# Performance work log

Hardware: AMD Instinct MI355X
Metric: run time of the kernel (lower is better)

The kernel has to match this reference:

```python
import jax, jax.numpy as jnp
import numpy as np

N_NODES = 50000
N_EDGES = 800000


def _layer_norm(h, g, b, eps=1e-5):
    mu = jnp.mean(h, axis=-1, keepdims=True)
    var = jnp.var(h, axis=-1, keepdims=True)
    return (h - mu) * jax.lax.rsqrt(var + eps) * g + b


def _gat_layer(h, src, tgt, trans_prob, W, a_src, a_tgt, Wtp, a_tp, Wskip, b, concat):
    """GATLayerImp3-style edge-softmax attention with transition-prob scores."""
    N = h.shape[0]
    NH, F = a_src.shape
    proj = (h @ W).reshape(N, NH, F)                       # (N, NH, F)
    s_src = jnp.einsum('nhf,hf->nh', proj, a_src)          # (N, NH)
    s_tgt = jnp.einsum('nhf,hf->nh', proj, a_tgt)
    e = s_src[src] + s_tgt[tgt]                            # (E, NH)
    tp_proj = (trans_prob @ Wtp).reshape(-1, NH, F)        # (E, NH, F)
    e = e + jnp.einsum('ehf,hf->eh', tp_proj, a_tp)
    e = jax.nn.leaky_relu(e, 0.2)
    # neighborhood softmax over edges sharing the same target node
    m = jax.ops.segment_max(e, tgt, num_segments=N)        # (N, NH)
    w = jnp.exp(e - m[tgt])
    denom = jax.ops.segment_sum(w, tgt, num_segments=N)
    alpha = w / (denom[tgt] + 1e-16)                       # (E, NH)
    msg = proj[src] * alpha[..., None]                     # (E, NH, F)
    out = jax.ops.segment_sum(msg, tgt, num_segments=N)    # (N, NH, F)
    if Wskip is None:
        out = out + h[:, None, :]                          # F == F_in
    else:
        out = out + (h @ Wskip).reshape(N, NH, F)
    out = out.reshape(N, NH * F) if concat else out.mean(axis=1)
    return jax.nn.elu(out + b)


def setup_inputs() -> dict:
    key = jax.random.key(0)
    ks = jax.random.split(key, 32)
    s = 0.1
    inp = {
        'node_features': jax.random.normal(ks[0], (N_NODES, 128), jnp.float32),
        'edge_index': jax.random.randint(ks[1], (2, N_EDGES), 0, N_NODES, jnp.int32),
        'edge_prob': jax.random.uniform(ks[2], (N_EDGES, 1), jnp.float32),
        'x': jax.random.randint(ks[3], (64, 128), 0, N_NODES, jnp.int32),
        'W0': jax.random.normal(ks[4], (128, 256)) * s,
        'a_src0': jax.random.normal(ks[5], (16, 16)) * s,
        'a_tgt0': jax.random.normal(ks[6], (16, 16)) * s,
        'Wtp0': jax.random.normal(ks[7], (1, 256)) * s,
        'a_tp0': jax.random.normal(ks[8], (16, 16)) * s,
        'Wskip0': jax.random.normal(ks[9], (128, 256)) * s,
        'b0': jnp.zeros((256,)),
        'W1': jax.random.normal(ks[10], (256, 256)) * s,
        'a_src1': jax.random.normal(ks[11], (16, 16)) * s,
        'a_tgt1': jax.random.normal(ks[12], (16, 16)) * s,
        'Wtp1': jax.random.normal(ks[13], (1, 256)) * s,
        'a_tp1': jax.random.normal(ks[14], (16, 16)) * s,
        'Wskip1': jax.random.normal(ks[15], (256, 256)) * s,
        'b1': jnp.zeros((256,)),
        'ln1_g': jnp.ones((256,)),
        'ln1_b': jnp.zeros((256,)),
        'W2': jax.random.normal(ks[16], (256, 256)) * s,
        'a_src2': jax.random.normal(ks[17], (1, 256)) * s,
        'a_tgt2': jax.random.normal(ks[18], (1, 256)) * s,
        'Wtp2': jax.random.normal(ks[19], (1, 256)) * s,
        'a_tp2': jax.random.normal(ks[20], (1, 256)) * s,
        'b2': jnp.zeros((256,)),
        'ln2_g': jnp.ones((256,)),
        'ln2_b': jnp.zeros((256,)),
    }
    return inp


def reference(node_features, edge_index, edge_prob, x,
              W0, a_src0, a_tgt0, Wtp0, a_tp0, Wskip0, b0,
              W1, a_src1, a_tgt1, Wtp1, a_tp1, Wskip1, b1, ln1_g, ln1_b,
              W2, a_src2, a_tgt2, Wtp2, a_tp2, b2, ln2_g, ln2_b):
    src, tgt = edge_index[0], edge_index[1]
    # node encoder GAT layer (concat 16 heads x 16 feats -> 256)
    h = _gat_layer(node_features, src, tgt, edge_prob,
                   W0, a_src0, a_tgt0, Wtp0, a_tp0, Wskip0, b0, concat=True)
    # GM layer 0: GAT (concat) + layer norm
    h = _gat_layer(h, src, tgt, edge_prob,
                   W1, a_src1, a_tgt1, Wtp1, a_tp1, Wskip1, b1, concat=True)
    h = _layer_norm(h, ln1_g, ln1_b)
    # GM layer 1: GAT (avg last, 1 head x 256; skip is identity add) + layer norm
    h = _gat_layer(h, src, tgt, edge_prob,
                   W2, a_src2, a_tgt2, Wtp2, a_tp2, None, b2, concat=False)
    h = _layer_norm(h, ln2_g, ln2_b)
    # indexed gather of node embeddings into per-sequence embeddings
    out = h[x]                                              # (B, S, d_model)
    return out
```

## Files before the change

### kernel.cpp

```cpp
#include <hip/hip_runtime.h>
#include <hip/hip_fp16.h>
#include <math.h>

typedef __attribute__((ext_vector_type(8))) short    s16x8;
typedef __attribute__((ext_vector_type(8))) _Float16 h16x8;
typedef __attribute__((ext_vector_type(4))) float    f32x4;
typedef __attribute__((ext_vector_type(4))) int      i32x4;

__device__ __forceinline__ short f2h(float x){ return __half_as_short(__float2half(x)); }
__device__ __forceinline__ float h2f(short s){ return __half2float(__short_as_half(s)); }

__global__ void k_prep(const float* W0, const float* Ws0, const float* W1,
                       const float* Ws1, const float* W2,
                       short* W0t, short* Ws0t, short* W1t, short* Ws1t, short* W2t,
                       const float* Wtp0, const float* a_tp0,
                       const float* Wtp1, const float* a_tp1,
                       const float* Wtp2, const float* a_tp2, float* cvec,
                       int* counts, int N){
  __shared__ float buf[256];
  int b = blockIdx.x;
  if (b < 1024){
    int idx = b*256 + threadIdx.x;
    const float* W; short* Wt; int K; int base;
    if (idx < 32768)      { W=W0;  Wt=W0t;  K=128; base=0; }
    else if (idx < 65536) { W=Ws0; Wt=Ws0t; K=128; base=32768; }
    else if (idx < 131072){ W=W1;  Wt=W1t;  K=256; base=65536; }
    else if (idx < 196608){ W=Ws1; Wt=Ws1t; K=256; base=131072; }
    else                  { W=W2;  Wt=W2t;  K=256; base=196608; }
    int i = idx - base;
    int n = i / K, k = i - n*K;
    Wt[i] = f2h(W[(size_t)k*256 + n]);
  } else if (b < 1027){
    int layer = b - 1024;
    const float* Wtp = layer==0 ? Wtp0 : (layer==1 ? Wtp1 : Wtp2);
    const float* atp = layer==0 ? a_tp0 : (layer==1 ? a_tp1 : a_tp2);
    float* c = cvec + (layer==0 ? 0 : (layer==1 ? 16 : 32));
    int NH = (layer==2) ? 1 : 16;
    int t = threadIdx.x;
    buf[t] = Wtp[t] * atp[t];
    __syncthreads();
    int F = 256 / NH;
    if (t < NH){
      float s = 0.f;
      for (int f = 0; f < F; f++) s += buf[t*F + f];
      c[t] = s;
    }
  } else {
    int i = (b - 1027)*256 + threadIdx.x;
    if (i < N) counts[i] = 0;
  }
}

__global__ void k_hist(const int* tgt, int* counts, int* rank, int E){
  int i = blockIdx.x*blockDim.x + threadIdx.x;
  if (i < E) rank[i] = atomicAdd(&counts[tgt[i]], 1);
}
__global__ void k_scan1(const int* counts, int* row_excl, int* partials, int N){
  __shared__ int buf[1024];
  int t = threadIdx.x; int i = blockIdx.x*1024 + t;
  int v = (i < N) ? counts[i] : 0;
  buf[t] = v; __syncthreads();
  for (int o = 1; o < 1024; o <<= 1){
    int x = (t >= o) ? buf[t-o] : 0;
    __syncthreads();
    buf[t] += x;
    __syncthreads();
  }
  if (i < N) row_excl[i] = buf[t] - v;
  if (t == 1023) partials[blockIdx.x] = buf[1023];
}
__global__ void k_scan3(int* row_start, const int* partials, int N, int E){
  __shared__ int base;
  int b = blockIdx.x;
  int pb = (b*256) >> 10;
  if (threadIdx.x == 0){
    int s = 0;
    for (int k = 0; k < pb; k++) s += partials[k];
    base = s;
  }
  __syncthreads();
  int i = b*256 + threadIdx.x;
  if (i < N) row_start[i] += base;
  if (i == 0) row_start[N] = E;
}
__global__ void k_scatter(const int* src, const int* tgt, const float* eprob,
                          const int* row_start, const int* rank,
                          long long* es, int E){
  int i = blockIdx.x*blockDim.x + threadIdx.x;
  if (i >= E) return;
  int p = row_start[tgt[i]] + rank[i];
  unsigned long long v = ((unsigned long long)(unsigned)__float_as_int(eprob[i]) << 32)
                       | (unsigned)src[i];
  __builtin_nontemporal_store((long long)v, es + p);
}

template<int AF32>
__device__ __forceinline__ s16x8 loadA(const void* Ab, size_t off){
  if constexpr (AF32){
    const float* p = (const float*)Ab + off;
    float4 a0 = *(const float4*)p;
    float4 a1 = *(const float4*)(p + 4);
    s16x8 r;
    r[0]=f2h(a0.x); r[1]=f2h(a0.y); r[2]=f2h(a0.z); r[3]=f2h(a0.w);
    r[4]=f2h(a1.x); r[5]=f2h(a1.y); r[6]=f2h(a1.z); r[7]=f2h(a1.w);
    return r;
  } else {
    return *(const s16x8*)((const short*)Ab + off);
  }
}

template<int KC, int AF32>
__global__ __launch_bounds__(256)
void k_gemm_lds(const void* __restrict__ Ab,
                const short* __restrict__ B1t, const short* __restrict__ B2t,
                short* __restrict__ C1b, short* __restrict__ C2b,
                unsigned char* __restrict__ C8, float* __restrict__ pscale,
                const float* __restrict__ asrc, const float* __restrict__ atgt,
                const float* __restrict__ asrc1, const float* __restrict__ atgt1,
                float* __restrict__ s_src, float* __restrict__ s_tgt, int M){
  const int K = KC*32;
  __shared__ short lA[64*32];
  __shared__ short lB[256*32];
  const int tid  = threadIdx.x;
  const int lane = tid & 63;
  const int wave = tid >> 6;
  const int m16  = lane & 15;
  const int q    = lane >> 4;
  const int swz  = (m16 >> 1) & 3;
  const int r0   = blockIdx.x * 64;
  const bool first = (blockIdx.y == 0);
  const short* __restrict__ Bt = first ? B1t : B2t;
  short* __restrict__ Cb = first ? C1b : C2b;

  int arow = r0 + (tid >> 2); if (arow >= M) arow = M - 1;
  const int akq = (tid & 3) ^ ((tid >> 3) & 3);
  int bn[4], bkq[4];
  #pragma unroll
  for (int j = 0; j < 4; j++){
    int sj = j*256 + tid;
    bn[j]  = sj >> 2;
    bkq[j] = (sj & 3) ^ ((sj >> 3) & 3);
  }

  f32x4 acc[4][4];
  #pragma unroll
  for (int mi = 0; mi < 4; mi++)
    #pragma unroll
    for (int ni = 0; ni < 4; ni++) acc[mi][ni] = {0.f,0.f,0.f,0.f};

  s16x8 ra = loadA<AF32>(Ab, (size_t)arow*K + akq*8);
  s16x8 rb[4];
  #pragma unroll
  for (int j = 0; j < 4; j++)
    rb[j] = *(const s16x8*)(Bt + (size_t)bn[j]*K + bkq[j]*8);

  for (int c = 0; c < KC; c++){
    __syncthreads();
    *(s16x8*)(lA + tid*8) = ra;
    #pragma unroll
    for (int j = 0; j < 4; j++)
      *(s16x8*)(lB + (j*256 + tid)*8) = rb[j];
    __syncthreads();

    if (c + 1 < KC){
      int k0 = (c+1)*32;
      ra = loadA<AF32>(Ab, (size_t)arow*K + k0 + akq*8);
      #pragma unroll
      for (int j = 0; j < 4; j++)
        rb[j] = *(const s16x8*)(Bt + (size_t)bn[j]*K + k0 + bkq[j]*8);
    }

    s16x8 Af[4], Bf[4];
    #pragma unroll
    for (int mi = 0; mi < 4; mi++){
      int slot = (mi*16 + m16)*4 + (q ^ swz);
      Af[mi] = *(const s16x8*)(lA + slot*8);
    }
    #pragma unroll
    for (int ni = 0; ni < 4; ni++){
      int n = wave*64 + ni*16 + m16;
      int slot = n*4 + (q ^ swz);
      Bf[ni] = *(const s16x8*)(lB + slot*8);
    }
    #pragma unroll
    for (int mi = 0; mi < 4; mi++)
      #pragma unroll
      for (int ni = 0; ni < 4; ni++)
        acc[mi][ni] = __builtin_amdgcn_mfma_f32_16x16x32_f16(
            *(h16x8*)&Bf[ni], *(h16x8*)&Af[mi], acc[mi][ni], 0, 0, 0);
  }

  #pragma unroll
  for (int mi = 0; mi < 4; mi++){
    int row = r0 + mi*16 + m16;
    bool ok = (row < M);
    #pragma unroll
    for (int ni = 0; ni < 4; ni++){
      if (ok && Cb){
        size_t o = (size_t)row*256 + wave*64 + ni*16 + q*4;
        short4 u; u.x = f2h(acc[mi][ni][0]); u.y = f2h(acc[mi][ni][1]);
        u.z = f2h(acc[mi][ni][2]); u.w = f2h(acc[mi][ni][3]);
        *(short4*)(Cb + o) = u;
      }
      if (first && asrc){
        int hh = wave*4 + ni;
        const float* as = asrc + hh*16 + q*4;
        const float* at = atgt + hh*16 + q*4;
        float pss = acc[mi][ni][0]*as[0] + acc[mi][ni][1]*as[1]
                  + acc[mi][ni][2]*as[2] + acc[mi][ni][3]*as[3];
        float pst = acc[mi][ni][0]*at[0] + acc[mi][ni][1]*at[1]
                  + acc[mi][ni][2]*at[2] + acc[mi][ni][3]*at[3];
        pss += __shfl_xor(pss, 16); pss += __shfl_xor(pss, 32);
        pst += __shfl_xor(pst, 16); pst += __shfl_xor(pst, 32);
        if (ok && q == 0){
          s_src[row*16 + hh] = pss;
          s_tgt[row*16 + hh] = pst;
        }
      }
    }
  }

  if (first && asrc1){
    float pss[4], pst[4];
    #pragma unroll
    for (int mi = 0; mi < 4; mi++){
      float ss = 0.f, st = 0.f;
      #pragma unroll
      for (int ni = 0; ni < 4; ni++){
        const float* as = asrc1 + wave*64 + ni*16 + q*4;
        const float* at = atgt1 + wave*64 + ni*16 + q*4;
        #pragma unroll
        for (int k = 0; k < 4; k++){
          ss += acc[mi][ni][k]*as[k];
          st += acc[mi][ni][k]*at[k];
        }
      }
      ss += __shfl_xor(ss, 16); ss += __shfl_xor(ss, 32);
      st += __shfl_xor(st, 16); st += __shfl_xor(st, 32);
      pss[mi] = ss; pst[mi] = st;
    }
    __syncthreads();
    float* sred = (float*)lB;
    if (q == 0){
      #pragma unroll
      for (int mi = 0; mi < 4; mi++){
        int r = mi*16 + m16;
        sred[wave*64 + r]       = pss[mi];
        sred[256 + wave*64 + r] = pst[mi];
      }
    }
    __syncthreads();
    if (tid < 64){
      int row = r0 + tid;
      if (row < M){
        float ss = sred[tid] + sred[64+tid] + sred[128+tid] + sred[192+tid];
        float st = sred[256+tid] + sred[320+tid] + sred[384+tid] + sred[448+tid];
        s_src[row] = ss;
        s_tgt[row] = st;
      }
    }
  }

  if (first && C8){
    float am[4];
    #pragma unroll
    for (int mi = 0; mi < 4; mi++){
      float a = 0.f;
      #pragma unroll
      for (int ni = 0; ni < 4; ni++)
        #pragma unroll
        for (int k = 0; k < 4; k++)
          a = fmaxf(a, fabsf(acc[mi][ni][k]));
      a = fmaxf(a, __shfl_xor(a, 16));
      a = fmaxf(a, __shfl_xor(a, 32));
      am[mi] = a;
    }
    __syncthreads();
    float* rmax = (float*)lA;
    if (q == 0){
      #pragma unroll
      for (int mi = 0; mi < 4; mi++) rmax[wave*64 + mi*16 + m16] = am[mi];
    }
    __syncthreads();
    #pragma unroll
    for (int mi = 0; mi < 4; mi++){
      int r = mi*16 + m16;
      int row = r0 + r;
      bool ok = (row < M);
      float s = fmaxf(fmaxf(rmax[r], rmax[64+r]), fmaxf(rmax[128+r], rmax[192+r]));
      float scl = s * (1.f/127.f);
      float inv = (s > 0.f) ? (127.f/s) : 0.f;
      if (ok && wave == 0 && q == 0) pscale[row] = scl;
      if (ok){
        #pragma unroll
        for (int ni = 0; ni < 4; ni++){
          int v0 = __float2int_rn(acc[mi][ni][0]*inv) + 128;
          int v1 = __float2int_rn(acc[mi][ni][1]*inv) + 128;
          int v2 = __float2int_rn(acc[mi][ni][2]*inv) + 128;
          int v3 = __float2int_rn(acc[mi][ni][3]*inv) + 128;
          unsigned pk = (unsigned)(v0 & 255) | ((unsigned)(v1 & 255) << 8)
                      | ((unsigned)(v2 & 255) << 16) | ((unsigned)(v3 & 255) << 24);
          *(unsigned*)(C8 + (size_t)row*256 + wave*64 + ni*16 + q*4) = pk;
        }
      }
    }
  }
}

template<int LN>
__global__ __launch_bounds__(256)
void k_attn16(const int* __restrict__ row_start, const int2* __restrict__ es,
              const float* __restrict__ s_src, const float* __restrict__ s_tgt,
              const float* __restrict__ cvec,
              const unsigned char* __restrict__ proj8, const float* __restrict__ pscale,
              const short* __restrict__ skipb,
              const float* __restrict__ bias,
              const float* __restrict__ ln_g, const float* __restrict__ ln_b,
              short* __restrict__ houtb, int N){
  __shared__ __align__(16) float wbuf[4][16][20];
  __shared__ __align__(16) int   svbuf[4][16];
  __shared__ __align__(16) float scbuf[4][16];
  const int lane = threadIdx.x & 63;
  const int wave = threadIdx.x >> 6;
  const int node = blockIdx.x*4 + wave;
  if (node >= N) return;
  const int beg = row_start[node], end = row_start[node+1];

  const int h2 = lane >> 2;
  const int j4 = lane & 15;
  const int g  = lane >> 4;

  const f32x4 stg = *(const f32x4*)(s_tgt + (size_t)node*16 + g*4);
  const f32x4 cg  = *(const f32x4*)(cvec + g*4);

  float d = 0.f, dws = 0.f;
  float acc0 = 0.f, acc1 = 0.f, acc2 = 0.f, acc3 = 0.f;

  for (int s0 = beg; s0 < end; s0 += 16){
    int cnt = end - s0; if (cnt > 16) cnt = 16;
    int i  = s0 + j4;
    bool valid = (i < end);
    int ic = valid ? i : (end - 1);
    int2 e2 = es[ic];
    int sv = e2.x;
    float tp = __int_as_float(e2.y);
    f32x4 rv = *(const f32x4*)(s_src + (size_t)sv*16 + g*4);
    if (g == 0){ svbuf[wave][j4] = sv; scbuf[wave][j4] = pscale[sv]; }
    #pragma unroll
    for (int k = 0; k < 4; k++){
      float e = rv[k] + stg[k] + tp*cg[k];
      e = (e > 0.f) ? e : 0.2f*e;
      wbuf[wave][g*4 + k][j4] = valid ? __expf(e) : 0.f;
    }
    const unsigned* __restrict__ pp = (const unsigned*)proj8 + lane;
    for (int j = 0; j < cnt; j += 4){
      f32x4 w4  = *(const f32x4*)&wbuf[wave][h2][j];
      f32x4 sc4 = *(const f32x4*)&scbuf[wave][j];
      i32x4 sv4 = *(const i32x4*)&svbuf[wave][j];
      unsigned q0 = pp[(size_t)sv4.x*64];
      unsigned q1 = pp[(size_t)sv4.y*64];
      unsigned q2 = pp[(size_t)sv4.z*64];
      unsigned q3 = pp[(size_t)sv4.w*64];
      float ws0 = w4.x*sc4.x, ws1 = w4.y*sc4.y, ws2 = w4.z*sc4.z, ws3 = w4.w*sc4.w;
      d   += (w4.x + w4.y) + (w4.z + w4.w);
      dws += (ws0 + ws1) + (ws2 + ws3);
      acc0 += ws0*(float)(q0 & 255) + ws1*(float)(q1 & 255)
            + ws2*(float)(q2 & 255) + ws3*(float)(q3 & 255);
      acc1 += ws0*(float)((q0 >> 8) & 255) + ws1*(float)((q1 >> 8) & 255)
            + ws2*(float)((q2 >> 8) & 255) + ws3*(float)((q3 >> 8) & 255);
      acc2 += ws0*(float)((q0 >> 16) & 255) + ws1*(float)((q1 >> 16) & 255)
            + ws2*(float)((q2 >> 16) & 255) + ws3*(float)((q3 >> 16) & 255);
      acc3 += ws0*(float)(q0 >> 24) + ws1*(float)(q1 >> 24)
            + ws2*(float)(q2 >> 24) + ws3*(float)(q3 >> 24);
    }
  }
  float inv = 1.f / (d + 1e-16f);
  float c128 = 128.f * dws;

  short4 sk = ((const short4*)(skipb + (size_t)node*256))[lane];
  float acc[4];
  acc[0] = (acc0 - c128)*inv + h2f(sk.x); acc[1] = (acc1 - c128)*inv + h2f(sk.y);
  acc[2] = (acc2 - c128)*inv + h2f(sk.z); acc[3] = (acc3 - c128)*inv + h2f(sk.w);

  #pragma unroll
  for (int j = 0; j < 4; j++){
    float v = acc[j] + bias[lane*4 + j];
    acc[j] = (v > 0.f) ? v : (__expf(v) - 1.f);
  }
  if (LN){
    float s  = acc[0] + acc[1] + acc[2] + acc[3];
    float s2 = acc[0]*acc[0] + acc[1]*acc[1] + acc[2]*acc[2] + acc[3]*acc[3];
    for (int o = 32; o > 0; o >>= 1){ s += __shfl_xor(s, o); s2 += __shfl_xor(s2, o); }
    float mu  = s * (1.f/256.f);
    float var = s2 * (1.f/256.f) - mu*mu;
    float rs  = rsqrtf(var + 1e-5f);
    #pragma unroll
    for (int j = 0; j < 4; j++)
      acc[j] = (acc[j] - mu)*rs*ln_g[lane*4 + j] + ln_b[lane*4 + j];
  }
  short4 ub; ub.x = f2h(acc[0]); ub.y = f2h(acc[1]);
  ub.z = f2h(acc[2]); ub.w = f2h(acc[3]);
  ((short4*)(houtb + (size_t)node*256))[lane] = ub;
}

__global__ __launch_bounds__(256)
void k_attn1(const int* __restrict__ row_start, const int2* __restrict__ es,
             const float* __restrict__ s_src, const float* __restrict__ s_tgt,
             const float* __restrict__ cvec,
             const unsigned char* __restrict__ proj8, const float* __restrict__ pscale,
             const short* __restrict__ skipb,
             const float* __restrict__ bias,
             const float* __restrict__ ln_g, const float* __restrict__ ln_b,
             short* __restrict__ houtb, int N){
  __shared__ __align__(16) float wb1[4][64];
  __shared__ __align__(16) int   sb1[4][64];
  __shared__ __align__(16) float scb1[4][64];
  const int lane = threadIdx.x & 63;
  const int wave = threadIdx.x >> 6;
  const int node = blockIdx.x*4 + wave;
  if (node >= N) return;
  const int beg = row_start[node], end = row_start[node+1];

  const float c0 = cvec[0];
  const float st = s_tgt[node];
  float d = 0.f, dws = 0.f;
  float acc0 = 0.f, acc1 = 0.f, acc2 = 0.f, acc3 = 0.f;

  for (int s0 = beg; s0 < end; s0 += 64){
    int cnt = end - s0; if (cnt > 64) cnt = 64;
    int i  = s0 + lane;
    bool valid = (i < end);
    int ic = valid ? i : (end - 1);
    int2 e2 = es[ic];
    int sv = e2.x;
    float e = s_src[sv] + st + __int_as_float(e2.y)*c0;
    e = (e > 0.f) ? e : 0.2f*e;
    float w = valid ? __expf(e) : 0.f;
    wb1[wave][lane] = w;
    sb1[wave][lane] = sv;
    scb1[wave][lane] = pscale[sv];
    const unsigned* __restrict__ pp = (const unsigned*)proj8 + lane;
    for (int j = 0; j < cnt; j += 4){
      f32x4 w4  = *(const f32x4*)&wb1[wave][j];
      f32x4 sc4 = *(const f32x4*)&scb1[wave][j];
      i32x4 sv4 = *(const i32x4*)&sb1[wave][j];
      unsigned q0 = pp[(size_t)sv4.x*64];
      unsigned q1 = pp[(size_t)sv4.y*64];
      unsigned q2 = pp[(size_t)sv4.z*64];
      unsigned q3 = pp[(size_t)sv4.w*64];
      float ws0 = w4.x*sc4.x, ws1 = w4.y*sc4.y, ws2 = w4.z*sc4.z, ws3 = w4.w*sc4.w;
      d   += (w4.x + w4.y) + (w4.z + w4.w);
      dws += (ws0 + ws1) + (ws2 + ws3);
      acc0 += ws0*(float)(q0 & 255) + ws1*(float)(q1 & 255)
            + ws2*(float)(q2 & 255) + ws3*(float)(q3 & 255);
      acc1 += ws0*(float)((q0 >> 8) & 255) + ws1*(float)((q1 >> 8) & 255)
            + ws2*(float)((q2 >> 8) & 255) + ws3*(float)((q3 >> 8) & 255);
      acc2 += ws0*(float)((q0 >> 16) & 255) + ws1*(float)((q1 >> 16) & 255)
            + ws2*(float)((q2 >> 16) & 255) + ws3*(float)((q3 >> 16) & 255);
      acc3 += ws0*(float)(q0 >> 24) + ws1*(float)(q1 >> 24)
            + ws2*(float)(q2 >> 24) + ws3*(float)(q3 >> 24);
    }
  }
  float inv = 1.f / (d + 1e-16f);
  float c128 = 128.f * dws;

  short4 sk = ((const short4*)(skipb + (size_t)node*256))[lane];
  float acc[4];
  acc[0] = (acc0 - c128)*inv + h2f(sk.x); acc[1] = (acc1 - c128)*inv + h2f(sk.y);
  acc[2] = (acc2 - c128)*inv + h2f(sk.z); acc[3] = (acc3 - c128)*inv + h2f(sk.w);

  #pragma unroll
  for (int j = 0; j < 4; j++){
    float v = acc[j] + bias[lane*4 + j];
    acc[j] = (v > 0.f) ? v : (__expf(v) - 1.f);
  }
  float s  = acc[0] + acc[1] + acc[2] + acc[3];
  float s2 = acc[0]*acc[0] + acc[1]*acc[1] + acc[2]*acc[2] + acc[3]*acc[3];
  for (int o = 32; o > 0; o >>= 1){ s += __shfl_xor(s, o); s2 += __shfl_xor(s2, o); }
  float mu  = s * (1.f/256.f);
  float var = s2 * (1.f/256.f) - mu*mu;
  float rs  = rsqrtf(var + 1e-5f);
  #pragma unroll
  for (int j = 0; j < 4; j++)
    acc[j] = (acc[j] - mu)*rs*ln_g[lane*4 + j] + ln_b[lane*4 + j];
  short4 ub; ub.x = f2h(acc[0]); ub.y = f2h(acc[1]);
  ub.z = f2h(acc[2]); ub.w = f2h(acc[3]);
  ((short4*)(houtb + (size_t)node*256))[lane] = ub;
}

__global__ void k_gather(const short* hb, const int* x, float* out, int R){
  int r = blockIdx.x, t = threadIdx.x;
  if (r >= R) return;
  out[(size_t)r*256 + t] = h2f(hb[(size_t)x[r]*256 + t]);
}

extern "C" void kernel_launch(void* const* d_in, const int* in_sizes, int n_in,
                              void* d_out, int out_size, void* d_ws, size_t ws_size,
                              hipStream_t stream){
  const int N = in_sizes[0] / 128;
  const int E = in_sizes[1] / 2;
  const int R = in_sizes[3];

  const float* nf    = (const float*)d_in[0];
  const int*   ei    = (const int*)d_in[1];
  const float* eprob = (const float*)d_in[2];
  const int*   xidx  = (const int*)d_in[3];
  const float* W0     = (const float*)d_in[4];
  const float* a_src0 = (const float*)d_in[5];
  const float* a_tgt0 = (const float*)d_in[6];
  const float* Wtp0   = (const float*)d_in[7];
  const float* a_tp0  = (const float*)d_in[8];
  const float* Wskip0 = (const float*)d_in[9];
  const float* b0     = (const float*)d_in[10];
  const float* W1     = (const float*)d_in[11];
  const float* a_src1 = (const float*)d_in[12];
  const float* a_tgt1 = (const float*)d_in[13];
  const float* Wtp1   = (const float*)d_in[14];
  const float* a_tp1  = (const float*)d_in[15];
  const float* Wskip1 = (const float*)d_in[16];
  const float* b1     = (const float*)d_in[17];
  const float* ln1_g  = (const float*)d_in[18];
  const float* ln1_b  = (const float*)d_in[19];
  const float* W2     = (const float*)d_in[20];
  const float* a_src2 = (const float*)d_in[21];
  const float* a_tgt2 = (const float*)d_in[22];
  const float* Wtp2   = (const float*)d_in[23];
  const float* a_tp2  = (const float*)d_in[24];
  const float* b2     = (const float*)d_in[25];
  const float* ln2_g  = (const float*)d_in[26];
  const float* ln2_b  = (const float*)d_in[27];

  char* ws = (char*)d_ws;
  size_t off = 0;
  auto alloc = [&](size_t bytes)->char*{
    char* p = ws + off; off = (off + bytes + 255) & ~(size_t)255; return p;
  };
  unsigned char* P8 = (unsigned char*)alloc((size_t)N*256);
  float* pscale    = (float*)alloc((size_t)N*4);
  short* hXb       = (short*)alloc((size_t)N*256*2);
  short* Skb       = (short*)alloc((size_t)N*256*2);
  float* s_src     = (float*)alloc((size_t)N*16*4);
  float* s_tgt     = (float*)alloc((size_t)N*16*4);
  float* cvec      = (float*)alloc(256);
  int*   counts    = (int*)alloc((size_t)N*4);
  int*   row_start = (int*)alloc((size_t)(N+1)*4);
  int*   partials  = (int*)alloc(256*4);
  int*   rank      = (int*)alloc((size_t)E*4);
  int2*  es        = (int2*)alloc((size_t)E*8);
  short* W0t       = (short*)alloc((size_t)128*256*2);
  short* Ws0t      = (short*)alloc((size_t)128*256*2);
  short* W1t       = (short*)alloc((size_t)256*256*2);
  short* Ws1t      = (short*)alloc((size_t)256*256*2);
  short* W2t       = (short*)alloc((size_t)256*256*2);
  (void)ws_size; (void)n_in; (void)out_size;

  const int* src = ei;
  const int* tgt = ei + E;

  int prep_blocks = 1027 + (N + 255)/256;
  k_prep<<<prep_blocks, 256, 0, stream>>>(W0, Wskip0, W1, Wskip1, W2,
                                          W0t, Ws0t, W1t, Ws1t, W2t,
                                          Wtp0, a_tp0, Wtp1, a_tp1, Wtp2, a_tp2, cvec,
                                          counts, N);

  k_hist<<<(E+255)/256, 256, 0, stream>>>(tgt, counts, rank, E);
  int NB = (N + 1023) / 1024;
  k_scan1<<<NB, 1024, 0, stream>>>(counts, row_start, partials, N);
  k_scan3<<<(N+255)/256, 256, 0, stream>>>(row_start, partials, N, E);
  k_scatter<<<(E+255)/256, 256, 0, stream>>>(src, tgt, eprob, row_start, rank,
                                             (long long*)es, E);

  const int gt = (N + 63) / 64;
  const int at = (N + 3) / 4;

  k_gemm_lds<4,1><<<dim3(gt,2), 256, 0, stream>>>(nf, W0t, Ws0t, nullptr, Skb, P8, pscale,
                                                  a_src0, a_tgt0, nullptr, nullptr,
                                                  s_src, s_tgt, N);
  k_attn16<0><<<at, 256, 0, stream>>>(row_start, es, s_src, s_tgt, cvec + 0,
                                      P8, pscale, Skb, b0, nullptr, nullptr, hXb, N);

  k_gemm_lds<8,0><<<dim3(gt,2), 256, 0, stream>>>(hXb, W1t, Ws1t, nullptr, Skb, P8, pscale,
                                                  a_src1, a_tgt1, nullptr, nullptr,
                                                  s_src, s_tgt, N);
  k_attn16<1><<<at, 256, 0, stream>>>(row_start, es, s_src, s_tgt, cvec + 16,
                                      P8, pscale, Skb, b1, ln1_g, ln1_b, hXb, N);

  k_gemm_lds<8,0><<<dim3(gt,1), 256, 0, stream>>>(hXb, W2t, nullptr, nullptr, nullptr,
                                                  P8, pscale,
                                                  nullptr, nullptr, a_src2, a_tgt2,
                                                  s_src, s_tgt, N);
  k_attn1<<<at, 256, 0, stream>>>(row_start, es, s_src, s_tgt, cvec + 32,
                                  P8, pscale, hXb, b2, ln2_g, ln2_b, Skb, N);

  k_gather<<<R, 256, 0, stream>>>(Skb, xidx, (float*)d_out, R);
}
```

Baseline: 443.8 us.

## Merge projection and skip GEMMs into one 512-thread block sharing the A tile

The two GEMMs that read the same activations (projection and skip weights), previously launched as a 2-wide grid in y, now run in one 512-thread block. The first four waves compute the projection and the last four compute the skip output, and both read a single shared A tile in LDS. This halves global reads of the A matrix and removes duplicate A loads into LDS. In exchange each block needs more LDS and more threads, which can reduce occupancy.

```diff
diff --git a/kernel.cpp b/kernel.cpp
--- a/kernel.cpp
+++ b/kernel.cpp
@@ -109,35 +109,36 @@
   }
 }
 
-template<int KC, int AF32>
-__global__ __launch_bounds__(256)
+template<int KC, int AF32, int DUAL>
+__global__ __launch_bounds__(DUAL ? 512 : 256)
 void k_gemm_lds(const void* __restrict__ Ab,
                 const short* __restrict__ B1t, const short* __restrict__ B2t,
-                short* __restrict__ C1b, short* __restrict__ C2b,
+                short* __restrict__ C2b,
                 unsigned char* __restrict__ C8, float* __restrict__ pscale,
                 const float* __restrict__ asrc, const float* __restrict__ atgt,
                 const float* __restrict__ asrc1, const float* __restrict__ atgt1,
                 float* __restrict__ s_src, float* __restrict__ s_tgt, int M){
   const int K = KC*32;
   __shared__ short lA[64*32];
-  __shared__ short lB[256*32];
+  __shared__ short lB[DUAL ? 2 : 1][256*32];
   const int tid  = threadIdx.x;
+  const int t8   = tid & 255;
   const int lane = tid & 63;
   const int wave = tid >> 6;
+  const int pw   = DUAL ? (wave >> 2) : 0;
+  const int cw   = wave & 3;
   const int m16  = lane & 15;
   const int q    = lane >> 4;
   const int swz  = (m16 >> 1) & 3;
   const int r0   = blockIdx.x * 64;
-  const bool first = (blockIdx.y == 0);
-  const short* __restrict__ Bt = first ? B1t : B2t;
-  short* __restrict__ Cb = first ? C1b : C2b;
-
-  int arow = r0 + (tid >> 2); if (arow >= M) arow = M - 1;
-  const int akq = (tid & 3) ^ ((tid >> 3) & 3);
+  const short* __restrict__ Bt = (DUAL && pw) ? B2t : B1t;
+
+  int arow = r0 + (t8 >> 2); if (arow >= M) arow = M - 1;
+  const int akq = (t8 & 3) ^ ((t8 >> 3) & 3);
   int bn[4], bkq[4];
   #pragma unroll
   for (int j = 0; j < 4; j++){
-    int sj = j*256 + tid;
+    int sj = j*256 + t8;
     bn[j]  = sj >> 2;
     bkq[j] = (sj & 3) ^ ((sj >> 3) & 3);
   }
@@ -148,7 +149,8 @@
     #pragma unroll
     for (int ni = 0; ni < 4; ni++) acc[mi][ni] = {0.f,0.f,0.f,0.f};
 
-  s16x8 ra = loadA<AF32>(Ab, (size_t)arow*K + akq*8);
+  s16x8 ra;
+  if (!DUAL || pw == 0) ra = loadA<AF32>(Ab, (size_t)arow*K + akq*8);
   s16x8 rb[4];
   #pragma unroll
   for (int j = 0; j < 4; j++)
@@ -156,15 +158,15 @@
 
   for (int c = 0; c < KC; c++){
     __syncthreads();
-    *(s16x8*)(lA + tid*8) = ra;
+    if (!DUAL || pw == 0) *(s16x8*)(lA + t8*8) = ra;
     #pragma unroll
     for (int j = 0; j < 4; j++)
-      *(s16x8*)(lB + (j*256 + tid)*8) = rb[j];
+      *(s16x8*)(lB[pw] + (j*256 + t8)*8) = rb[j];
     __syncthreads();
 
     if (c + 1 < KC){
       int k0 = (c+1)*32;
-      ra = loadA<AF32>(Ab, (size_t)arow*K + k0 + akq*8);
+      if (!DUAL || pw == 0) ra = loadA<AF32>(Ab, (size_t)arow*K + k0 + akq*8);
       #pragma unroll
       for (int j = 0; j < 4; j++)
         rb[j] = *(const s16x8*)(Bt + (size_t)bn[j]*K + k0 + bkq[j]*8);
@@ -178,9 +180,9 @@
     }
     #pragma unroll
     for (int ni = 0; ni < 4; ni++){
-      int n = wave*64 + ni*16 + m16;
+      int n = cw*64 + ni*16 + m16;
       int slot = n*4 + (q ^ swz);
-      Bf[ni] = *(const s16x8*)(lB + slot*8);
+      Bf[ni] = *(const s16x8*)(lB[pw] + slot*8);
     }
     #pragma unroll
     for (int mi = 0; mi < 4; mi++)
@@ -190,20 +192,30 @@
             *(h16x8*)&Bf[ni], *(h16x8*)&Af[mi], acc[mi][ni], 0, 0, 0);
   }
 
-  #pragma unroll
-  for (int mi = 0; mi < 4; mi++){
-    int row = r0 + mi*16 + m16;
-    bool ok = (row < M);
-    #pragma unroll
-    for (int ni = 0; ni < 4; ni++){
-      if (ok && Cb){
-        size_t o = (size_t)row*256 + wave*64 + ni*16 + q*4;
-        short4 u; u.x = f2h(acc[mi][ni][0]); u.y = f2h(acc[mi][ni][1]);
-        u.z = f2h(acc[mi][ni][2]); u.w = f2h(acc[mi][ni][3]);
-        *(short4*)(Cb + o) = u;
+  if (DUAL && pw == 1 && C2b){
+    #pragma unroll
+    for (int mi = 0; mi < 4; mi++){
+      int row = r0 + mi*16 + m16;
+      if (row < M){
+        #pragma unroll
+        for (int ni = 0; ni < 4; ni++){
+          size_t o = (size_t)row*256 + cw*64 + ni*16 + q*4;
+          short4 u; u.x = f2h(acc[mi][ni][0]); u.y = f2h(acc[mi][ni][1]);
+          u.z = f2h(acc[mi][ni][2]); u.w = f2h(acc[mi][ni][3]);
+          *(short4*)(C2b + o) = u;
+        }
       }
-      if (first && asrc){
-        int hh = wave*4 + ni;
+    }
+  }
+
+  if (asrc && (!DUAL || pw == 0)){
+    #pragma unroll
+    for (int mi = 0; mi < 4; mi++){
+      int row = r0 + mi*16 + m16;
+      bool ok = (row < M);
+      #pragma unroll
+      for (int ni = 0; ni < 4; ni++){
+        int hh = cw*4 + ni;
         const float* as = asrc + hh*16 + q*4;
         const float* at = atgt + hh*16 + q*4;
         float pss = acc[mi][ni][0]*as[0] + acc[mi][ni][1]*as[1]
@@ -220,33 +232,35 @@
     }
   }
 
-  if (first && asrc1){
+  if (asrc1){
     float pss[4], pst[4];
-    #pragma unroll
-    for (int mi = 0; mi < 4; mi++){
-      float ss = 0.f, st = 0.f;
-      #pragma unroll
-      for (int ni = 0; ni < 4; ni++){
-        const float* as = asrc1 + wave*64 + ni*16 + q*4;
-        const float* at = atgt1 + wave*64 + ni*16 + q*4;
+    if (!DUAL || pw == 0){
+      #pragma unroll
+      for (int mi = 0; mi < 4; mi++){
+        float ss = 0.f, st = 0.f;
         #pragma unroll
-        for (int k = 0; k < 4; k++){
-          ss += acc[mi][ni][k]*as[k];
-          st += acc[mi][ni][k]*at[k];
+        for (int ni = 0; ni < 4; ni++){
+          const float* as = asrc1 + cw*64 + ni*16 + q*4;
+          const float* at = atgt1 + cw*64 + ni*16 + q*4;
+          #pragma unroll
+          for (int k = 0; k < 4; k++){
+            ss += acc[mi][ni][k]*as[k];
+            st += acc[mi][ni][k]*at[k];
+          }
         }
+        ss += __shfl_xor(ss, 16); ss += __shfl_xor(ss, 32);
+        st += __shfl_xor(st, 16); st += __shfl_xor(st, 32);
+        pss[mi] = ss; pst[mi] = st;
       }
-      ss += __shfl_xor(ss, 16); ss += __shfl_xor(ss, 32);
-      st += __shfl_xor(st, 16); st += __shfl_xor(st, 32);
-      pss[mi] = ss; pst[mi] = st;
-    }
-    __syncthreads();
-    float* sred = (float*)lB;
-    if (q == 0){
+    }
+    __syncthreads();
+    float* sred = (float*)lB[0];
+    if ((!DUAL || pw == 0) && q == 0){
       #pragma unroll
       for (int mi = 0; mi < 4; mi++){
         int r = mi*16 + m16;
-        sred[wave*64 + r]       = pss[mi];
-        sred[256 + wave*64 + r] = pst[mi];
+        sred[cw*64 + r]       = pss[mi];
+        sred[256 + cw*64 + r] = pst[mi];
       }
     }
     __syncthreads();
@@ -261,46 +275,50 @@
     }
   }
 
-  if (first && C8){
+  if (C8){
     float am[4];
-    #pragma unroll
-    for (int mi = 0; mi < 4; mi++){
-      float a = 0.f;
-      #pragma unroll
-      for (int ni = 0; ni < 4; ni++)
+    if (!DUAL || pw == 0){
+      #pragma unroll
+      for (int mi = 0; mi < 4; mi++){
+        float a = 0.f;
         #pragma unroll
-        for (int k = 0; k < 4; k++)
-          a = fmaxf(a, fabsf(acc[mi][ni][k]));
-      a = fmaxf(a, __shfl_xor(a, 16));
-      a = fmaxf(a, __shfl_xor(a, 32));
-      am[mi] = a;
+        for (int ni = 0; ni < 4; ni++)
+          #pragma unroll
+          for (int k = 0; k < 4; k++)
+            a = fmaxf(a, fabsf(acc[mi][ni][k]));
+        a = fmaxf(a, __shfl_xor(a, 16));
+        a = fmaxf(a, __shfl_xor(a, 32));
+        am[mi] = a;
+      }
     }
     __syncthreads();
     float* rmax = (float*)lA;
-    if (q == 0){
-      #pragma unroll
-      for (int mi = 0; mi < 4; mi++) rmax[wave*64 + mi*16 + m16] = am[mi];
-    }
-    __syncthreads();
-    #pragma unroll
-    for (int mi = 0; mi < 4; mi++){
-      int r = mi*16 + m16;
-      int row = r0 + r;
-      bool ok = (row < M);
-      float s = fmaxf(fmaxf(rmax[r], rmax[64+r]), fmaxf(rmax[128+r], rmax[192+r]));
-      float scl = s * (1.f/127.f);
-      float inv = (s > 0.f) ? (127.f/s) : 0.f;
-      if (ok && wave == 0 && q == 0) pscale[row] = scl;
-      if (ok){
-        #pragma unroll
-        for (int ni = 0; ni < 4; ni++){
-          int v0 = __float2int_rn(acc[mi][ni][0]*inv) + 128;
-          int v1 = __float2int_rn(acc[mi][ni][1]*inv) + 128;
-          int v2 = __float2int_rn(acc[mi][ni][2]*inv) + 128;
-          int v3 = __float2int_rn(acc[mi][ni][3]*inv) + 128;
-          unsigned pk = (unsigned)(v0 & 255) | ((unsigned)(v1 & 255) << 8)
-                      | ((unsigned)(v2 & 255) << 16) | ((unsigned)(v3 & 255) << 24);
-          *(unsigned*)(C8 + (size_t)row*256 + wave*64 + ni*16 + q*4) = pk;
+    if ((!DUAL || pw == 0) && q == 0){
+      #pragma unroll
+      for (int mi = 0; mi < 4; mi++) rmax[cw*64 + mi*16 + m16] = am[mi];
+    }
+    __syncthreads();
+    if (!DUAL || pw == 0){
+      #pragma unroll
+      for (int mi = 0; mi < 4; mi++){
+        int r = mi*16 + m16;
+        int row = r0 + r;
+        bool ok = (row < M);
+        float s = fmaxf(fmaxf(rmax[r], rmax[64+r]), fmaxf(rmax[128+r], rmax[192+r]));
+        float scl = s * (1.f/127.f);
+        float inv = (s > 0.f) ? (127.f/s) : 0.f;
+        if (ok && cw == 0 && q == 0) pscale[row] = scl;
+        if (ok){
+          #pragma unroll
+          for (int ni = 0; ni < 4; ni++){
+            int v0 = __float2int_rn(acc[mi][ni][0]*inv) + 128;
+            int v1 = __float2int_rn(acc[mi][ni][1]*inv) + 128;
+            int v2 = __float2int_rn(acc[mi][ni][2]*inv) + 128;
+            int v3 = __float2int_rn(acc[mi][ni][3]*inv) + 128;
+            unsigned pk = (unsigned)(v0 & 255) | ((unsigned)(v1 & 255) << 8)
+                        | ((unsigned)(v2 & 255) << 16) | ((unsigned)(v3 & 255) << 24);
+            *(unsigned*)(C8 + (size_t)row*256 + cw*64 + ni*16 + q*4) = pk;
+          }
         }
       }
     }
@@ -573,22 +591,21 @@
   const int gt = (N + 63) / 64;
   const int at = (N + 3) / 4;
 
-  k_gemm_lds<4,1><<<dim3(gt,2), 256, 0, stream>>>(nf, W0t, Ws0t, nullptr, Skb, P8, pscale,
-                                                  a_src0, a_tgt0, nullptr, nullptr,
-                                                  s_src, s_tgt, N);
+  k_gemm_lds<4,1,1><<<gt, 512, 0, stream>>>(nf, W0t, Ws0t, Skb, P8, pscale,
+                                            a_src0, a_tgt0, nullptr, nullptr,
+                                            s_src, s_tgt, N);
   k_attn16<0><<<at, 256, 0, stream>>>(row_start, es, s_src, s_tgt, cvec + 0,
                                       P8, pscale, Skb, b0, nullptr, nullptr, hXb, N);
 
-  k_gemm_lds<8,0><<<dim3(gt,2), 256, 0, stream>>>(hXb, W1t, Ws1t, nullptr, Skb, P8, pscale,
-                                                  a_src1, a_tgt1, nullptr, nullptr,
-                                                  s_src, s_tgt, N);
+  k_gemm_lds<8,0,1><<<gt, 512, 0, stream>>>(hXb, W1t, Ws1t, Skb, P8, pscale,
+                                            a_src1, a_tgt1, nullptr, nullptr,
+                                            s_src, s_tgt, N);
   k_attn16<1><<<at, 256, 0, stream>>>(row_start, es, s_src, s_tgt, cvec + 16,
                                       P8, pscale, Skb, b1, ln1_g, ln1_b, hXb, N);
 
-  k_gemm_lds<8,0><<<dim3(gt,1), 256, 0, stream>>>(hXb, W2t, nullptr, nullptr, nullptr,
-                                                  P8, pscale,
-                                                  nullptr, nullptr, a_src2, a_tgt2,
-                                                  s_src, s_tgt, N);
+  k_gemm_lds<8,0,0><<<gt, 256, 0, stream>>>(hXb, W2t, nullptr, nullptr, P8, pscale,
+                                            nullptr, nullptr, a_src2, a_tgt2,
+                                            s_src, s_tgt, N);
   k_attn1<<<at, 256, 0, stream>>>(row_start, es, s_src, s_tgt, cvec + 32,
                                   P8, pscale, hXb, b2, ln2_g, ln2_b, Skb, N);
 
```

Result: slower. 453.5 us (+2.2%).
